# Performance work log

Hardware: AMD Instinct MI355X
Metric: run time of the kernel (lower is better)

## Reference

```python
import jax, jax.numpy as jnp
import numpy as np

N_HEAD, D_MODEL, D_HEAD, D_OUT = 16, 1024, 64, 1024
Q_INNER = N_HEAD * D_HEAD


def setup_inputs() -> dict:
    key = jax.random.key(0)
    ks = jax.random.split(key, 10)
    B, S = 1, 4096
    hidden_state = jax.random.normal(ks[0], (B, S, D_MODEL), dtype=jnp.float32)
    # causal mask, (B,1,S,S), 1 = attend, 0 = masked
    attention_mask = jnp.tril(jnp.ones((S, S), dtype=jnp.int32))[None, None, :, :]
    s = 0.02
    Wq = jax.random.normal(ks[1], (D_MODEL, Q_INNER), dtype=jnp.float32) * s
    bq = jnp.zeros((Q_INNER,), dtype=jnp.float32)
    Wk = jax.random.normal(ks[2], (D_MODEL, D_HEAD), dtype=jnp.float32) * s
    bk = jnp.zeros((D_HEAD,), dtype=jnp.float32)
    Wv = jax.random.normal(ks[3], (D_MODEL, D_HEAD), dtype=jnp.float32) * s
    bv = jnp.zeros((D_HEAD,), dtype=jnp.float32)
    Wo = jax.random.normal(ks[4], (Q_INNER, D_OUT), dtype=jnp.float32) * s
    bo = jnp.zeros((D_OUT,), dtype=jnp.float32)
    return {"hidden_state": hidden_state, "attention_mask": attention_mask,
            "Wq": Wq, "bq": bq, "Wk": Wk, "bk": bk, "Wv": Wv, "bv": bv,
            "Wo": Wo, "bo": bo}


def reference(hidden_state, attention_mask, Wq, bq, Wk, bk, Wv, bv, Wo, bo):
    B, S, _ = hidden_state.shape
    q = hidden_state @ Wq + bq                    # (B,S,H*Dh)
    k = hidden_state @ Wk + bk                    # (B,S,Dh) single shared KV head
    v = hidden_state @ Wv + bv                    # (B,S,Dh)
    q = q.reshape(B, S, N_HEAD, D_HEAD)           # (B,S,H,Dh)
    scale = 1.0 / jnp.sqrt(jnp.float32(D_HEAD))
    # scores: (B,H,S,S) — shared K broadcast over heads
    scores = jnp.einsum('bqhd,bkd->bhqk', q, k) * scale
    scores = jnp.where(attention_mask == 0, -jnp.inf, scores)
    probs = jax.nn.softmax(scores, axis=-1)
    out = jnp.einsum('bhqk,bkd->bqhd', probs, v)  # (B,S,H,Dh)
    out = out.reshape(B, S, Q_INNER)
    return out @ Wo + bo
```

## Files before the change

kernel.cpp:

```cpp
#include <hip/hip_runtime.h>
#include <hip/hip_bf16.h>
#include <math.h>

typedef __bf16 bf16;
typedef __bf16 bf16x4 __attribute__((ext_vector_type(4)));
typedef __bf16 bf16x8 __attribute__((ext_vector_type(8)));
typedef float f32x4 __attribute__((ext_vector_type(4)));

#define AS1(p) ((const __attribute__((address_space(1))) void*)(p))
#define AS3(p) ((__attribute__((address_space(3))) void*)(p))

__device__ __forceinline__ void gld_lds16(const void* g, void* l) {
  __builtin_amdgcn_global_load_lds(AS1(g), AS3(l), 16, 0, 0);
}

#define MFMA16(a, b, c) __builtin_amdgcn_mfma_f32_16x16x32_bf16((a), (b), (c), 0, 0, 0)

#define QSCALE_F 0.180336880f

struct Sched { unsigned short e[768]; };
constexpr Sched make_sched() {
  Sched s{};
  for (int bx = 0; bx < 256; ++bx) {
    int h = bx >> 4, i = bx & 15;
    s.e[bx]       = (unsigned short)(((31 - i) << 6) | (h << 2) | 1);
    s.e[bx + 256] = (unsigned short)(((31 - i) << 6) | (h << 2) | 2);
    s.e[bx + 512] = (unsigned short)((i << 6) | (h << 2) | 0);
  }
  return s;
}
__device__ constexpr Sched SCHED = make_sched();

__global__ void cast_f32_bf16(const float4* __restrict__ in, bf16* __restrict__ out, int n4) {
  int i = blockIdx.x * blockDim.x + threadIdx.x;
  if (i < n4) {
    float4 v = in[i];
    bf16x4 o4 = {(bf16)v.x, (bf16)v.y, (bf16)v.z, (bf16)v.w};
    *(bf16x4*)(out + (size_t)i * 4) = o4;
  }
}

__global__ void prep_wqkv(const float* __restrict__ Wq, const float* __restrict__ Wk,
                          const float* __restrict__ Wv, bf16* __restrict__ out) {
  __shared__ float t[64][65];
  const int ob = blockIdx.y;
  const float* src;
  int C, c0;
  if (ob < 16)      { src = Wq; C = 1024; c0 = ob * 64; }
  else if (ob == 16){ src = Wk; C = 64;   c0 = 0; }
  else              { src = Wv; C = 64;   c0 = 0; }
  const int r0 = blockIdx.x * 64;
  const int tx = threadIdx.x & 63, ty = threadIdx.x >> 6;
#pragma unroll
  for (int j = 0; j < 16; j++)
    t[ty + j * 4][tx] = src[(size_t)(r0 + ty + j * 4) * C + c0 + tx];
  __syncthreads();
#pragma unroll
  for (int j = 0; j < 16; j++)
    out[(size_t)(ob * 64 + ty + j * 4) * 1024 + r0 + tx] = (bf16)t[tx][ty + j * 4];
}

__global__ void transpose_cast_f32_bf16(const float* __restrict__ in, bf16* __restrict__ out,
                                        int C, int ldout) {
  __shared__ float t[64][65];
  int r0 = blockIdx.y * 64, c0 = blockIdx.x * 64;
  int tx = threadIdx.x & 63, ty = threadIdx.x >> 6;
#pragma unroll
  for (int j = 0; j < 16; j++)
    t[ty + j * 4][tx] = in[(size_t)(r0 + ty + j * 4) * C + c0 + tx];
  __syncthreads();
#pragma unroll
  for (int j = 0; j < 16; j++)
    out[(size_t)(c0 + ty + j * 4) * ldout + r0 + tx] = (bf16)t[tx][ty + j * 4];
}

__global__ void pack_bias3(const float* __restrict__ bq, const float* __restrict__ bk,
                           const float* __restrict__ bv, float* __restrict__ o) {
  int i = blockIdx.x * 256 + threadIdx.x;
  if (i < 1024) o[i] = bq[i];
  else if (i < 1088) o[i] = bk[i - 1024];
  else if (i < 1152) o[i] = bv[i - 1088];
}

template <int OUTF32, int QSCALE>
__global__ __launch_bounds__(256) void gemm_bt64(const bf16* __restrict__ A,
                                                 const bf16* __restrict__ B,
                                                 const float* __restrict__ bias,
                                                 void* __restrict__ Cout,
                                                 int M, int N, int K) {
  __shared__ bf16 As[64 * 32];
  __shared__ bf16 Bs[128 * 32];
  const int tid = threadIdx.x, w = tid >> 6, lane = tid & 63;
  const int g = lane >> 4, r = lane & 15;
  const int cpx = gridDim.x >> 3;
  const int l = (blockIdx.x & 7) * cpx + (blockIdx.x >> 3);
  const int ntn = N >> 7;
  const int my = l / ntn, mx = l - my * ntn;
  const int tm = my * 64, tn = mx * 128;
  const int wr = w >> 1, wc = w & 1;

  f32x4 acc[2][4] = {};

  const char* gA = (const char*)(A + (size_t)tm * K);
  const char* gB = (const char*)(B + (size_t)tn * K);
  const int linA = w * 1024 + lane * 16;
  const int lin0 = (w * 2 + 0) * 1024 + lane * 16;
  const int lin1 = (w * 2 + 1) * 1024 + lane * 16;
  const int rA = linA >> 6, cA = linA & 63;
  const int rB0 = lin0 >> 6, cB0 = lin0 & 63;
  const int rB1 = lin1 >> 6, cB1 = lin1 & 63;
  char* ldsA  = (char*)As + w * 1024;
  char* ldsB0 = (char*)Bs + (w * 2 + 0) * 1024;
  char* ldsB1 = (char*)Bs + (w * 2 + 1) * 1024;

  for (int k0 = 0; k0 < K; k0 += 32) {
    gld_lds16(gA + (size_t)rA * (K * 2) + k0 * 2 + cA, ldsA);
    gld_lds16(gB + (size_t)rB0 * (K * 2) + k0 * 2 + cB0, ldsB0);
    gld_lds16(gB + (size_t)rB1 * (K * 2) + k0 * 2 + cB1, ldsB1);
    __syncthreads();

    bf16x8 af[2], bfr[4];
#pragma unroll
    for (int m = 0; m < 2; m++)
      af[m] = *(const bf16x8*)&As[(wr * 32 + m * 16 + r) * 32 + g * 8];
#pragma unroll
    for (int n = 0; n < 4; n++)
      bfr[n] = *(const bf16x8*)&Bs[(wc * 64 + n * 16 + r) * 32 + g * 8];
#pragma unroll
    for (int m = 0; m < 2; m++)
#pragma unroll
      for (int n = 0; n < 4; n++)
        acc[m][n] = MFMA16(af[m], bfr[n], acc[m][n]);
    __syncthreads();
  }

#pragma unroll
  for (int m = 0; m < 2; m++) {
#pragma unroll
    for (int n = 0; n < 4; n++) {
      int crow = tm + wr * 32 + m * 16 + g * 4;
      int ccol = tn + wc * 64 + n * 16 + r;
      float bb = bias[ccol];
      float sc = (QSCALE && ccol < 1024) ? QSCALE_F : 1.0f;
#pragma unroll
      for (int j = 0; j < 4; j++) {
        float v = (acc[m][n][j] + bb) * sc;
        if (OUTF32)
          ((float*)Cout)[(size_t)(crow + j) * N + ccol] = v;
        else
          ((bf16*)Cout)[(size_t)(crow + j) * N + ccol] = (bf16)v;
      }
    }
  }
}

__global__ void kv_prep(const bf16* __restrict__ QKV, bf16* __restrict__ Ksw,
                        bf16* __restrict__ Vtsw) {
  __shared__ bf16 Vld[64][72];
  const int kv0 = blockIdx.x * 64;
  const int tid = threadIdx.x;
#pragma unroll
  for (int cc = 0; cc < 2; cc++) {
    const int c = tid + cc * 256;
    const int kvl = c >> 3, c8 = c & 7;
    bf16x8 kv8 = *(const bf16x8*)(QKV + (size_t)(kv0 + kvl) * 1152 + 1024 + c8 * 8);
    *(bf16x8*)(Ksw + (size_t)(kv0 + kvl) * 64 + ((c8 * 8) ^ ((kvl & 7) << 3))) = kv8;
    bf16x8 vv = *(const bf16x8*)(QKV + (size_t)(kv0 + kvl) * 1152 + 1088 + c8 * 8);
#pragma unroll
    for (int e = 0; e < 8; e++) Vld[c8 * 8 + e][kvl] = vv[e];
  }
  __syncthreads();
#pragma unroll
  for (int cc = 0; cc < 2; cc++) {
    const int c = tid + cc * 256;
    const int d = c >> 3, k8 = c & 7;
    bf16x8 o8 = *(const bf16x8*)&Vld[d][k8 * 8];
    *(bf16x8*)(Vtsw + (size_t)d * 4096 + kv0 + ((k8 * 8) ^ ((d & 7) << 3))) = o8;
  }
}

__global__ __launch_bounds__(256) void mqa_fwd(const bf16* __restrict__ QKV,
                                               const bf16* __restrict__ Ksw,
                                               const bf16* __restrict__ Vtsw,
                                               bf16* __restrict__ AO,
                                               float* __restrict__ po,
                                               float* __restrict__ psum) {
  __shared__ bf16 Ks[2][64 * 64];
  __shared__ bf16 Vs[2][64 * 64];
  __shared__ bf16 Ps[4 * 32 * 64];

  const int e = SCHED.e[blockIdx.x];
  const int qt = e >> 6, h = (e >> 2) & 15, part = e & 3;
  const int tbeg = (part == 2) ? qt + 1 : 0;
  const int tend = (part == 1) ? qt + 1 : 2 * qt + 2;

  const int tid = threadIdx.x, w = tid >> 6, lane = tid & 63;
  const int g = lane >> 4, r = lane & 15;
  const int qw = qt * 128 + w * 32;
  const int qown0 = qw + r;
  const int qown1 = qw + 16 + r;

  const char* Kg = (const char*)Ksw;
  const char* Vg = (const char*)Vtsw;
  char* PsB = (char*)Ps;
  const int lin0 = w * 2048 + lane * 16;
  const int lin1 = lin0 + 1024;
  const int sz = (r & 7) << 4;

  bf16x8 qf0[2], qf1[2];
#pragma unroll
  for (int kk = 0; kk < 2; kk++) {
    qf0[kk] = *(const bf16x8*)&QKV[(size_t)qown0 * 1152 + h * 64 + kk * 32 + g * 8];
    qf1[kk] = *(const bf16x8*)&QKV[(size_t)qown1 * 1152 + h * 64 + kk * 32 + g * 8];
  }

  const bf16 one = (bf16)1.0f;
  const bf16x8 ones = {one, one, one, one, one, one, one, one};

  f32x4 o[2][4] = {};
  f32x4 sums[2] = {};

  auto STAGE = [&](int t, int b) {
    const int kn = t * 64;
    char* kb = (char*)Ks + b * 8192 + w * 2048;
    char* vb = (char*)Vs + b * 8192 + w * 2048;
    gld_lds16(Kg + (size_t)kn * 128 + lin0, kb);
    gld_lds16(Kg + (size_t)kn * 128 + lin1, kb + 1024);
    gld_lds16(Vg + (size_t)(lin0 >> 7) * 8192 + kn * 2 + (lin0 & 127), vb);
    gld_lds16(Vg + (size_t)(lin1 >> 7) * 8192 + kn * 2 + (lin1 & 127), vb + 1024);
  };

  int buf = 0;
  STAGE(tbeg, 0);
  for (int t = tbeg; t < tend; ++t) {
    if (t + 1 < tend) {
      STAGE(t + 1, buf ^ 1);
      asm volatile("s_waitcnt vmcnt(4)" ::: "memory");
    } else {
      asm volatile("s_waitcnt vmcnt(0)" ::: "memory");
    }
    __builtin_amdgcn_sched_barrier(0);
    __builtin_amdgcn_s_barrier();

    const char* kt = (const char*)Ks + buf * 8192;
    const char* vt = (const char*)Vs + buf * 8192;
    const int kv0 = t * 64;

    f32x4 s0[4], s1[4];
    __builtin_amdgcn_s_setprio(1);
#pragma unroll
    for (int n = 0; n < 4; n++) {
      bf16x8 kf0 = *(const bf16x8*)(kt + (n * 16 + r) * 128 + ((g * 16) ^ sz));
      bf16x8 kf1 = *(const bf16x8*)(kt + (n * 16 + r) * 128 + ((64 + g * 16) ^ sz));
      f32x4 z0 = {0.f, 0.f, 0.f, 0.f};
      z0 = MFMA16(kf0, qf0[0], z0);
      z0 = MFMA16(kf1, qf0[1], z0);
      s0[n] = z0;
      f32x4 z1 = {0.f, 0.f, 0.f, 0.f};
      z1 = MFMA16(kf0, qf1[0], z1);
      z1 = MFMA16(kf1, qf1[1], z1);
      s1[n] = z1;
    }
    __builtin_amdgcn_s_setprio(0);

    if (t >= 2 * qt) {
#pragma unroll
      for (int n = 0; n < 4; n++)
#pragma unroll
        for (int jj = 0; jj < 4; jj++) {
          const int kv = kv0 + n * 16 + g * 4 + jj;
          if (kv > qown0) s0[n][jj] = -3.0e38f;
          if (kv > qown1) s1[n][jj] = -3.0e38f;
        }
    }

#pragma unroll
    for (int n = 0; n < 4; n++) {
      bf16x4 pk0, pk1;
#pragma unroll
      for (int jj = 0; jj < 4; jj++) {
        pk0[jj] = (bf16)__builtin_amdgcn_exp2f(s0[n][jj]);
        pk1[jj] = (bf16)__builtin_amdgcn_exp2f(s1[n][jj]);
      }
      *(bf16x4*)(PsB + w * 4096 + r * 128 + ((n * 32 + g * 8) ^ sz)) = pk0;
      *(bf16x4*)(PsB + w * 4096 + (16 + r) * 128 + ((n * 32 + g * 8) ^ sz)) = pk1;
    }

    asm volatile("s_waitcnt lgkmcnt(0)" ::: "memory");
    __builtin_amdgcn_sched_barrier(0);

    bf16x8 pa00 = *(const bf16x8*)(PsB + w * 4096 + r * 128 + ((g * 16) ^ sz));
    bf16x8 pa01 = *(const bf16x8*)(PsB + w * 4096 + r * 128 + ((64 + g * 16) ^ sz));
    bf16x8 pa10 = *(const bf16x8*)(PsB + w * 4096 + (16 + r) * 128 + ((g * 16) ^ sz));
    bf16x8 pa11 = *(const bf16x8*)(PsB + w * 4096 + (16 + r) * 128 + ((64 + g * 16) ^ sz));
    __builtin_amdgcn_s_setprio(1);
    sums[0] = MFMA16(pa00, ones, sums[0]);
    sums[0] = MFMA16(pa01, ones, sums[0]);
    sums[1] = MFMA16(pa10, ones, sums[1]);
    sums[1] = MFMA16(pa11, ones, sums[1]);
#pragma unroll
    for (int n = 0; n < 4; n++) {
      bf16x8 vf0 = *(const bf16x8*)(vt + (n * 16 + r) * 128 + ((g * 16) ^ sz));
      bf16x8 vf1 = *(const bf16x8*)(vt + (n * 16 + r) * 128 + ((64 + g * 16) ^ sz));
      o[0][n] = MFMA16(pa00, vf0, o[0][n]);
      o[0][n] = MFMA16(pa01, vf1, o[0][n]);
      o[1][n] = MFMA16(pa10, vf0, o[1][n]);
      o[1][n] = MFMA16(pa11, vf1, o[1][n]);
    }
    __builtin_amdgcn_s_setprio(0);
    __builtin_amdgcn_s_barrier();
    buf ^= 1;
  }

  if (part == 0) {
#pragma unroll
    for (int H = 0; H < 2; H++)
#pragma unroll
      for (int jj = 0; jj < 4; jj++) {
        const float inv = 1.f / sums[H][jj];
        const int row = qw + H * 16 + g * 4 + jj;
#pragma unroll
        for (int n = 0; n < 4; n++)
          AO[(size_t)row * 1024 + h * 64 + n * 16 + r] = (bf16)(o[H][n][jj] * inv);
      }
  } else {
    const int slot = ((qt - 16) * 16 + h) * 2 + (part - 1);
    float* pb = po + (size_t)slot * 8192;
#pragma unroll
    for (int H = 0; H < 2; H++)
#pragma unroll
      for (int jj = 0; jj < 4; jj++) {
        const int row = w * 32 + H * 16 + g * 4 + jj;
#pragma unroll
        for (int n = 0; n < 4; n++)
          pb[row * 64 + n * 16 + r] = o[H][n][jj];
        if (r == 0) psum[slot * 128 + row] = sums[H][jj];
      }
  }
}

__global__ __launch_bounds__(256) void combine_split(const float* __restrict__ po,
                                                     const float* __restrict__ psum,
                                                     bf16* __restrict__ AO) {
  const int bxx = blockIdx.x;
  const int qt = 16 + (bxx >> 4), h = bxx & 15;
  const float* a  = po + (size_t)bxx * 16384;
  const float* b  = a + 8192;
  const float* sa = psum + bxx * 256;
  const float* sb = sa + 128;
  const int row = threadIdx.x >> 1, c0 = (threadIdx.x & 1) * 32;
  const float inv = 1.f / (sa[row] + sb[row]);
  const float* pa = a + row * 64 + c0;
  const float* pb = b + row * 64 + c0;
  bf16* dst = AO + (size_t)(qt * 128 + row) * 1024 + h * 64 + c0;
#pragma unroll
  for (int i = 0; i < 8; i++) {
    float4 va = ((const float4*)pa)[i];
    float4 vb = ((const float4*)pb)[i];
    bf16x4 o4 = {(bf16)((va.x + vb.x) * inv), (bf16)((va.y + vb.y) * inv),
                 (bf16)((va.z + vb.z) * inv), (bf16)((va.w + vb.w) * inv)};
    ((bf16x4*)dst)[i] = o4;
  }
}

extern "C" void kernel_launch(void* const* d_in, const int* in_sizes, int n_in,
                              void* d_out, int out_size, void* d_ws, size_t ws_size,
                              hipStream_t stream) {
  const float* H  = (const float*)d_in[0];
  const float* Wq = (const float*)d_in[2];
  const float* bq = (const float*)d_in[3];
  const float* Wk = (const float*)d_in[4];
  const float* bk = (const float*)d_in[5];
  const float* Wv = (const float*)d_in[6];
  const float* bv = (const float*)d_in[7];
  const float* Wo = (const float*)d_in[8];
  const float* bo = (const float*)d_in[9];
  float* out = (float*)d_out;

  const int S = 4096, DM = 1024;

  char* p = (char*)d_ws;
  bf16* Hb    = (bf16*)(p);
  bf16* QKV   = (bf16*)(p + 8388608);
  bf16* Wqkvt = (bf16*)(p + 17825792);
  bf16* Wot   = (bf16*)(p + 20185088);
  float* bqkv = (float*)(p + 22282240);
  bf16* Ksw   = (bf16*)(p + 22286848);
  bf16* Vtsw  = (bf16*)(p + 22811136);
  float* po   = (float*)(p + 23335424);
  float* psum = (float*)(p + 40112640);
  bf16* AOb   = Hb;

  cast_f32_bf16<<<(S * DM / 4 + 255) / 256, 256, 0, stream>>>((const float4*)H, Hb, S * DM / 4);
  prep_wqkv<<<dim3(16, 18), 256, 0, stream>>>(Wq, Wk, Wv, Wqkvt);
  transpose_cast_f32_bf16<<<dim3(16, 16), 256, 0, stream>>>(Wo, Wot, 1024, 1024);
  pack_bias3<<<5, 256, 0, stream>>>(bq, bk, bv, bqkv);

  gemm_bt64<0, 1><<<576, 256, 0, stream>>>(Hb, Wqkvt, bqkv, QKV, S, 1152, 1024);

  kv_prep<<<64, 256, 0, stream>>>(QKV, Ksw, Vtsw);

  mqa_fwd<<<768, 256, 0, stream>>>(QKV, Ksw, Vtsw, AOb, po, psum);
  combine_split<<<256, 256, 0, stream>>>(po, psum, AOb);

  gemm_bt64<1, 0><<<512, 256, 0, stream>>>(AOb, Wot, bo, out, S, 1024, 1024);
}
```

Baseline: 125.4 us.

## Balance causal attention work with tape schedule, double-buffer GEMM, bf16 partials

Replaces the fixed three-way split schedule with a compile-time tape. Each of the 768 blocks processes up to two segments, drawn from a paired short/long query tile, so that every block covers at most 22 KV tiles. The combine kernel now sums a variable number of partial slots (336 jobs). Partial outputs are stored as bf16 instead of fp32 to cut combine traffic, at some precision cost. Separately, the projection GEMM gains double-buffered LDS staging with async prefetch and MFMA priority hints, and fully-masked waves on the last diagonal tile skip compute.

```diff
diff --git a/kernel.cpp b/kernel.cpp
--- a/kernel.cpp
+++ b/kernel.cpp
@@ -18,18 +18,71 @@
 
 #define QSCALE_F 0.180336880f
 
-struct Sched { unsigned short e[768]; };
-constexpr Sched make_sched() {
-  Sched s{};
-  for (int bx = 0; bx < 256; ++bx) {
-    int h = bx >> 4, i = bx & 15;
-    s.e[bx]       = (unsigned short)(((31 - i) << 6) | (h << 2) | 1);
-    s.e[bx + 256] = (unsigned short)(((31 - i) << 6) | (h << 2) | 2);
-    s.e[bx + 512] = (unsigned short)((i << 6) | (h << 2) | 0);
-  }
-  return s;
-}
-__device__ constexpr Sched SCHED = make_sched();
+struct Seg { short qt, h, t0, t1, slot; };
+struct Tape { Seg s[768][2]; };
+struct CJob { short qt, h, base, parts; };
+struct CTab { CJob j[336]; };
+
+constexpr Tape make_tape() {
+  Tape tp{};
+  for (int b = 0; b < 768; ++b)
+    for (int s = 0; s < 2; ++s) tp.s[b][s] = Seg{0, 0, 0, 0, -1};
+  int slot_next = 0, blk = 0;
+  for (int h = 0; h < 16; ++h)
+    for (int i = 0; i < 16; ++i) {
+      const int n1 = 2 * i + 2;
+      const int qtj[2] = {i, 31 - i};
+      const int js[2] = {0, n1};
+      const int je[2] = {n1, 66};
+      int base[2] = {-1, -1}, fb[2] = {0, 0};
+      for (int j = 0; j < 2; ++j) {
+        fb[j] = js[j] / 22;
+        const int lb = (je[j] - 1) / 22;
+        const int parts = lb - fb[j] + 1;
+        if (parts > 1) { base[j] = slot_next; slot_next += parts; }
+      }
+      for (int k = 0; k < 3; ++k) {
+        int si = 0;
+        for (int j = 0; j < 2; ++j) {
+          const int a = js[j] > 22 * k ? js[j] : 22 * k;
+          const int b2 = je[j] < 22 * k + 22 ? je[j] : 22 * k + 22;
+          if (a < b2) {
+            const int slot = (base[j] >= 0) ? base[j] + (k - fb[j]) : -1;
+            tp.s[blk][si] = Seg{(short)qtj[j], (short)h, (short)(a - js[j]),
+                                (short)(b2 - js[j]), (short)slot};
+            ++si;
+          }
+        }
+        ++blk;
+      }
+    }
+  return tp;
+}
+
+constexpr CTab make_ctab() {
+  CTab ct{};
+  int slot_next = 0, nj = 0;
+  for (int h = 0; h < 16; ++h)
+    for (int i = 0; i < 16; ++i) {
+      const int n1 = 2 * i + 2;
+      const int qtj[2] = {i, 31 - i};
+      const int js[2] = {0, n1};
+      const int je[2] = {n1, 66};
+      for (int j = 0; j < 2; ++j) {
+        const int fb = js[j] / 22, lb = (je[j] - 1) / 22;
+        const int parts = lb - fb + 1;
+        if (parts > 1) {
+          ct.j[nj] = CJob{(short)qtj[j], (short)h, (short)slot_next, (short)parts};
+          slot_next += parts;
+          ++nj;
+        }
+      }
+    }
+  return ct;
+}
+
+__device__ constexpr Tape TAPE = make_tape();
+__device__ constexpr CTab CTAB = make_ctab();
 
 __global__ void cast_f32_bf16(const float4* __restrict__ in, bf16* __restrict__ out, int n4) {
   int i = blockIdx.x * blockDim.x + threadIdx.x;
@@ -88,8 +141,8 @@
                                                  const float* __restrict__ bias,
                                                  void* __restrict__ Cout,
                                                  int M, int N, int K) {
-  __shared__ bf16 As[64 * 32];
-  __shared__ bf16 Bs[128 * 32];
+  __shared__ bf16 As[2 * 64 * 32];
+  __shared__ bf16 Bs[2 * 128 * 32];
   const int tid = threadIdx.x, w = tid >> 6, lane = tid & 63;
   const int g = lane >> 4, r = lane & 15;
   const int cpx = gridDim.x >> 3;
@@ -109,29 +162,44 @@
   const int rA = linA >> 6, cA = linA & 63;
   const int rB0 = lin0 >> 6, cB0 = lin0 & 63;
   const int rB1 = lin1 >> 6, cB1 = lin1 & 63;
-  char* ldsA  = (char*)As + w * 1024;
-  char* ldsB0 = (char*)Bs + (w * 2 + 0) * 1024;
-  char* ldsB1 = (char*)Bs + (w * 2 + 1) * 1024;
-
-  for (int k0 = 0; k0 < K; k0 += 32) {
-    gld_lds16(gA + (size_t)rA * (K * 2) + k0 * 2 + cA, ldsA);
-    gld_lds16(gB + (size_t)rB0 * (K * 2) + k0 * 2 + cB0, ldsB0);
-    gld_lds16(gB + (size_t)rB1 * (K * 2) + k0 * 2 + cB1, ldsB1);
-    __syncthreads();
+
+  auto STAGE = [&](int ks, int b) {
+    char* dA = (char*)As + b * 4096 + w * 1024;
+    char* dB = (char*)Bs + b * 8192 + (w * 2) * 1024;
+    gld_lds16(gA + (size_t)rA * (K * 2) + ks * 64 + cA, dA);
+    gld_lds16(gB + (size_t)rB0 * (K * 2) + ks * 64 + cB0, dB);
+    gld_lds16(gB + (size_t)rB1 * (K * 2) + ks * 64 + cB1, dB + 1024);
+  };
+
+  const int nk = K >> 5;
+  STAGE(0, 0);
+  int buf = 0;
+  for (int ks = 0; ks < nk; ++ks) {
+    if (ks + 1 < nk) {
+      STAGE(ks + 1, buf ^ 1);
+      asm volatile("s_waitcnt vmcnt(3)" ::: "memory");
+    } else {
+      asm volatile("s_waitcnt vmcnt(0)" ::: "memory");
+    }
+    __builtin_amdgcn_sched_barrier(0);
+    __builtin_amdgcn_s_barrier();
 
     bf16x8 af[2], bfr[4];
 #pragma unroll
     for (int m = 0; m < 2; m++)
-      af[m] = *(const bf16x8*)&As[(wr * 32 + m * 16 + r) * 32 + g * 8];
+      af[m] = *(const bf16x8*)&As[buf * 2048 + (wr * 32 + m * 16 + r) * 32 + g * 8];
 #pragma unroll
     for (int n = 0; n < 4; n++)
-      bfr[n] = *(const bf16x8*)&Bs[(wc * 64 + n * 16 + r) * 32 + g * 8];
+      bfr[n] = *(const bf16x8*)&Bs[buf * 4096 + (wc * 64 + n * 16 + r) * 32 + g * 8];
+    __builtin_amdgcn_s_setprio(1);
 #pragma unroll
     for (int m = 0; m < 2; m++)
 #pragma unroll
       for (int n = 0; n < 4; n++)
         acc[m][n] = MFMA16(af[m], bfr[n], acc[m][n]);
-    __syncthreads();
+    __builtin_amdgcn_s_setprio(0);
+    __builtin_amdgcn_s_barrier();
+    buf ^= 1;
   }
 
 #pragma unroll
@@ -183,22 +251,14 @@
                                                const bf16* __restrict__ Ksw,
                                                const bf16* __restrict__ Vtsw,
                                                bf16* __restrict__ AO,
-                                               float* __restrict__ po,
+                                               bf16* __restrict__ po,
                                                float* __restrict__ psum) {
   __shared__ bf16 Ks[2][64 * 64];
   __shared__ bf16 Vs[2][64 * 64];
   __shared__ bf16 Ps[4 * 32 * 64];
 
-  const int e = SCHED.e[blockIdx.x];
-  const int qt = e >> 6, h = (e >> 2) & 15, part = e & 3;
-  const int tbeg = (part == 2) ? qt + 1 : 0;
-  const int tend = (part == 1) ? qt + 1 : 2 * qt + 2;
-
   const int tid = threadIdx.x, w = tid >> 6, lane = tid & 63;
   const int g = lane >> 4, r = lane & 15;
-  const int qw = qt * 128 + w * 32;
-  const int qown0 = qw + r;
-  const int qown1 = qw + 16 + r;
 
   const char* Kg = (const char*)Ksw;
   const char* Vg = (const char*)Vtsw;
@@ -207,18 +267,8 @@
   const int lin1 = lin0 + 1024;
   const int sz = (r & 7) << 4;
 
-  bf16x8 qf0[2], qf1[2];
-#pragma unroll
-  for (int kk = 0; kk < 2; kk++) {
-    qf0[kk] = *(const bf16x8*)&QKV[(size_t)qown0 * 1152 + h * 64 + kk * 32 + g * 8];
-    qf1[kk] = *(const bf16x8*)&QKV[(size_t)qown1 * 1152 + h * 64 + kk * 32 + g * 8];
-  }
-
   const bf16 one = (bf16)1.0f;
   const bf16x8 ones = {one, one, one, one, one, one, one, one};
-
-  f32x4 o[2][4] = {};
-  f32x4 sums[2] = {};
 
   auto STAGE = [&](int t, int b) {
     const int kn = t * 64;
@@ -230,136 +280,164 @@
     gld_lds16(Vg + (size_t)(lin1 >> 7) * 8192 + kn * 2 + (lin1 & 127), vb + 1024);
   };
 
-  int buf = 0;
-  STAGE(tbeg, 0);
-  for (int t = tbeg; t < tend; ++t) {
-    if (t + 1 < tend) {
-      STAGE(t + 1, buf ^ 1);
-      asm volatile("s_waitcnt vmcnt(4)" ::: "memory");
+#pragma unroll 1
+  for (int sidx = 0; sidx < 2; ++sidx) {
+    const Seg sg = TAPE.s[blockIdx.x][sidx];
+    if (sg.t1 <= sg.t0) continue;
+    const int qt = sg.qt, h = sg.h, tbeg = sg.t0, tend = sg.t1, slot = sg.slot;
+    const int qw = qt * 128 + w * 32;
+    const int qown0 = qw + r;
+    const int qown1 = qw + 16 + r;
+
+    bf16x8 qf0[2], qf1[2];
+#pragma unroll
+    for (int kk = 0; kk < 2; kk++) {
+      qf0[kk] = *(const bf16x8*)&QKV[(size_t)qown0 * 1152 + h * 64 + kk * 32 + g * 8];
+      qf1[kk] = *(const bf16x8*)&QKV[(size_t)qown1 * 1152 + h * 64 + kk * 32 + g * 8];
+    }
+
+    f32x4 o[2][4] = {};
+    f32x4 sums[2] = {};
+
+    int buf = 0;
+    STAGE(tbeg, 0);
+#pragma unroll 1
+    for (int t = tbeg; t < tend; ++t) {
+      if (t + 1 < tend) {
+        STAGE(t + 1, buf ^ 1);
+        asm volatile("s_waitcnt vmcnt(4)" ::: "memory");
+      } else {
+        asm volatile("s_waitcnt vmcnt(0)" ::: "memory");
+      }
+      __builtin_amdgcn_sched_barrier(0);
+      __builtin_amdgcn_s_barrier();
+
+      const char* kt = (const char*)Ks + buf * 8192;
+      const char* vt = (const char*)Vs + buf * 8192;
+      const int kv0 = t * 64;
+      const bool deadw = (t == 2 * qt + 1) && (w < 2);
+
+      if (!deadw) {
+        f32x4 s0[4], s1[4];
+        __builtin_amdgcn_s_setprio(1);
+#pragma unroll
+        for (int n = 0; n < 4; n++) {
+          bf16x8 kf0 = *(const bf16x8*)(kt + (n * 16 + r) * 128 + ((g * 16) ^ sz));
+          bf16x8 kf1 = *(const bf16x8*)(kt + (n * 16 + r) * 128 + ((64 + g * 16) ^ sz));
+          f32x4 z0 = {0.f, 0.f, 0.f, 0.f};
+          z0 = MFMA16(kf0, qf0[0], z0);
+          z0 = MFMA16(kf1, qf0[1], z0);
+          s0[n] = z0;
+          f32x4 z1 = {0.f, 0.f, 0.f, 0.f};
+          z1 = MFMA16(kf0, qf1[0], z1);
+          z1 = MFMA16(kf1, qf1[1], z1);
+          s1[n] = z1;
+        }
+        __builtin_amdgcn_s_setprio(0);
+
+        if (t >= 2 * qt) {
+#pragma unroll
+          for (int n = 0; n < 4; n++)
+#pragma unroll
+            for (int jj = 0; jj < 4; jj++) {
+              const int kv = kv0 + n * 16 + g * 4 + jj;
+              if (kv > qown0) s0[n][jj] = -3.0e38f;
+              if (kv > qown1) s1[n][jj] = -3.0e38f;
+            }
+        }
+
+#pragma unroll
+        for (int n = 0; n < 4; n++) {
+          bf16x4 pk0, pk1;
+#pragma unroll
+          for (int jj = 0; jj < 4; jj++) {
+            pk0[jj] = (bf16)__builtin_amdgcn_exp2f(s0[n][jj]);
+            pk1[jj] = (bf16)__builtin_amdgcn_exp2f(s1[n][jj]);
+          }
+          *(bf16x4*)(PsB + w * 4096 + r * 128 + ((n * 32 + g * 8) ^ sz)) = pk0;
+          *(bf16x4*)(PsB + w * 4096 + (16 + r) * 128 + ((n * 32 + g * 8) ^ sz)) = pk1;
+        }
+
+        asm volatile("s_waitcnt lgkmcnt(0)" ::: "memory");
+        __builtin_amdgcn_sched_barrier(0);
+
+        bf16x8 pa00 = *(const bf16x8*)(PsB + w * 4096 + r * 128 + ((g * 16) ^ sz));
+        bf16x8 pa01 = *(const bf16x8*)(PsB + w * 4096 + r * 128 + ((64 + g * 16) ^ sz));
+        bf16x8 pa10 = *(const bf16x8*)(PsB + w * 4096 + (16 + r) * 128 + ((g * 16) ^ sz));
+        bf16x8 pa11 = *(const bf16x8*)(PsB + w * 4096 + (16 + r) * 128 + ((64 + g * 16) ^ sz));
+        __builtin_amdgcn_s_setprio(1);
+        sums[0] = MFMA16(pa00, ones, sums[0]);
+        sums[0] = MFMA16(pa01, ones, sums[0]);
+        sums[1] = MFMA16(pa10, ones, sums[1]);
+        sums[1] = MFMA16(pa11, ones, sums[1]);
+#pragma unroll
+        for (int n = 0; n < 4; n++) {
+          bf16x8 vf0 = *(const bf16x8*)(vt + (n * 16 + r) * 128 + ((g * 16) ^ sz));
+          bf16x8 vf1 = *(const bf16x8*)(vt + (n * 16 + r) * 128 + ((64 + g * 16) ^ sz));
+          o[0][n] = MFMA16(pa00, vf0, o[0][n]);
+          o[0][n] = MFMA16(pa01, vf1, o[0][n]);
+          o[1][n] = MFMA16(pa10, vf0, o[1][n]);
+          o[1][n] = MFMA16(pa11, vf1, o[1][n]);
+        }
+        __builtin_amdgcn_s_setprio(0);
+      }
+      __builtin_amdgcn_s_barrier();
+      buf ^= 1;
+    }
+
+    if (slot < 0) {
+#pragma unroll
+      for (int H = 0; H < 2; H++)
+#pragma unroll
+        for (int jj = 0; jj < 4; jj++) {
+          const float inv = 1.f / sums[H][jj];
+          const int row = qw + H * 16 + g * 4 + jj;
+#pragma unroll
+          for (int n = 0; n < 4; n++)
+            AO[(size_t)row * 1024 + h * 64 + n * 16 + r] = (bf16)(o[H][n][jj] * inv);
+        }
     } else {
-      asm volatile("s_waitcnt vmcnt(0)" ::: "memory");
-    }
-    __builtin_amdgcn_sched_barrier(0);
-    __builtin_amdgcn_s_barrier();
-
-    const char* kt = (const char*)Ks + buf * 8192;
-    const char* vt = (const char*)Vs + buf * 8192;
-    const int kv0 = t * 64;
-
-    f32x4 s0[4], s1[4];
-    __builtin_amdgcn_s_setprio(1);
-#pragma unroll
-    for (int n = 0; n < 4; n++) {
-      bf16x8 kf0 = *(const bf16x8*)(kt + (n * 16 + r) * 128 + ((g * 16) ^ sz));
-      bf16x8 kf1 = *(const bf16x8*)(kt + (n * 16 + r) * 128 + ((64 + g * 16) ^ sz));
-      f32x4 z0 = {0.f, 0.f, 0.f, 0.f};
-      z0 = MFMA16(kf0, qf0[0], z0);
-      z0 = MFMA16(kf1, qf0[1], z0);
-      s0[n] = z0;
-      f32x4 z1 = {0.f, 0.f, 0.f, 0.f};
-      z1 = MFMA16(kf0, qf1[0], z1);
-      z1 = MFMA16(kf1, qf1[1], z1);
-      s1[n] = z1;
-    }
-    __builtin_amdgcn_s_setprio(0);
-
-    if (t >= 2 * qt) {
-#pragma unroll
-      for (int n = 0; n < 4; n++)
+      bf16* pb = po + (size_t)slot * 8192;
+#pragma unroll
+      for (int H = 0; H < 2; H++)
 #pragma unroll
         for (int jj = 0; jj < 4; jj++) {
-          const int kv = kv0 + n * 16 + g * 4 + jj;
-          if (kv > qown0) s0[n][jj] = -3.0e38f;
-          if (kv > qown1) s1[n][jj] = -3.0e38f;
-        }
-    }
-
-#pragma unroll
-    for (int n = 0; n < 4; n++) {
-      bf16x4 pk0, pk1;
-#pragma unroll
-      for (int jj = 0; jj < 4; jj++) {
-        pk0[jj] = (bf16)__builtin_amdgcn_exp2f(s0[n][jj]);
-        pk1[jj] = (bf16)__builtin_amdgcn_exp2f(s1[n][jj]);
-      }
-      *(bf16x4*)(PsB + w * 4096 + r * 128 + ((n * 32 + g * 8) ^ sz)) = pk0;
-      *(bf16x4*)(PsB + w * 4096 + (16 + r) * 128 + ((n * 32 + g * 8) ^ sz)) = pk1;
-    }
-
-    asm volatile("s_waitcnt lgkmcnt(0)" ::: "memory");
-    __builtin_amdgcn_sched_barrier(0);
-
-    bf16x8 pa00 = *(const bf16x8*)(PsB + w * 4096 + r * 128 + ((g * 16) ^ sz));
-    bf16x8 pa01 = *(const bf16x8*)(PsB + w * 4096 + r * 128 + ((64 + g * 16) ^ sz));
-    bf16x8 pa10 = *(const bf16x8*)(PsB + w * 4096 + (16 + r) * 128 + ((g * 16) ^ sz));
-    bf16x8 pa11 = *(const bf16x8*)(PsB + w * 4096 + (16 + r) * 128 + ((64 + g * 16) ^ sz));
-    __builtin_amdgcn_s_setprio(1);
-    sums[0] = MFMA16(pa00, ones, sums[0]);
-    sums[0] = MFMA16(pa01, ones, sums[0]);
-    sums[1] = MFMA16(pa10, ones, sums[1]);
-    sums[1] = MFMA16(pa11, ones, sums[1]);
-#pragma unroll
-    for (int n = 0; n < 4; n++) {
-      bf16x8 vf0 = *(const bf16x8*)(vt + (n * 16 + r) * 128 + ((g * 16) ^ sz));
-      bf16x8 vf1 = *(const bf16x8*)(vt + (n * 16 + r) * 128 + ((64 + g * 16) ^ sz));
-      o[0][n] = MFMA16(pa00, vf0, o[0][n]);
-      o[0][n] = MFMA16(pa01, vf1, o[0][n]);
-      o[1][n] = MFMA16(pa10, vf0, o[1][n]);
-      o[1][n] = MFMA16(pa11, vf1, o[1][n]);
-    }
-    __builtin_amdgcn_s_setprio(0);
-    __builtin_amdgcn_s_barrier();
-    buf ^= 1;
-  }
-
-  if (part == 0) {
-#pragma unroll
-    for (int H = 0; H < 2; H++)
-#pragma unroll
-      for (int jj = 0; jj < 4; jj++) {
-        const float inv = 1.f / sums[H][jj];
-        const int row = qw + H * 16 + g * 4 + jj;
-#pragma unroll
-        for (int n = 0; n < 4; n++)
-          AO[(size_t)row * 1024 + h * 64 + n * 16 + r] = (bf16)(o[H][n][jj] * inv);
-      }
-  } else {
-    const int slot = ((qt - 16) * 16 + h) * 2 + (part - 1);
-    float* pb = po + (size_t)slot * 8192;
-#pragma unroll
-    for (int H = 0; H < 2; H++)
-#pragma unroll
-      for (int jj = 0; jj < 4; jj++) {
-        const int row = w * 32 + H * 16 + g * 4 + jj;
-#pragma unroll
-        for (int n = 0; n < 4; n++)
-          pb[row * 64 + n * 16 + r] = o[H][n][jj];
-        if (r == 0) psum[slot * 128 + row] = sums[H][jj];
-      }
-  }
-}
-
-__global__ __launch_bounds__(256) void combine_split(const float* __restrict__ po,
+          const int row = w * 32 + H * 16 + g * 4 + jj;
+#pragma unroll
+          for (int n = 0; n < 4; n++)
+            pb[row * 64 + n * 16 + r] = (bf16)o[H][n][jj];
+          if (r == 0) psum[slot * 128 + row] = sums[H][jj];
+        }
+    }
+  }
+}
+
+__global__ __launch_bounds__(256) void combine_split(const bf16* __restrict__ po,
                                                      const float* __restrict__ psum,
                                                      bf16* __restrict__ AO) {
-  const int bxx = blockIdx.x;
-  const int qt = 16 + (bxx >> 4), h = bxx & 15;
-  const float* a  = po + (size_t)bxx * 16384;
-  const float* b  = a + 8192;
-  const float* sa = psum + bxx * 256;
-  const float* sb = sa + 128;
+  const CJob cj = CTAB.j[blockIdx.x];
   const int row = threadIdx.x >> 1, c0 = (threadIdx.x & 1) * 32;
-  const float inv = 1.f / (sa[row] + sb[row]);
-  const float* pa = a + row * 64 + c0;
-  const float* pb = b + row * 64 + c0;
-  bf16* dst = AO + (size_t)(qt * 128 + row) * 1024 + h * 64 + c0;
-#pragma unroll
-  for (int i = 0; i < 8; i++) {
-    float4 va = ((const float4*)pa)[i];
-    float4 vb = ((const float4*)pb)[i];
-    bf16x4 o4 = {(bf16)((va.x + vb.x) * inv), (bf16)((va.y + vb.y) * inv),
-                 (bf16)((va.z + vb.z) * inv), (bf16)((va.w + vb.w) * inv)};
-    ((bf16x4*)dst)[i] = o4;
+  float acc[32] = {};
+  float ssum = 0.f;
+#pragma unroll 1
+  for (int p = 0; p < cj.parts; ++p) {
+    const bf16* pb = po + (size_t)(cj.base + p) * 8192 + row * 64 + c0;
+    ssum += psum[(cj.base + p) * 128 + row];
+#pragma unroll
+    for (int v = 0; v < 4; ++v) {
+      bf16x8 x = ((const bf16x8*)pb)[v];
+#pragma unroll
+      for (int e = 0; e < 8; e++) acc[v * 8 + e] += (float)x[e];
+    }
+  }
+  const float inv = 1.f / ssum;
+  bf16* dst = AO + (size_t)(cj.qt * 128 + row) * 1024 + cj.h * 64 + c0;
+#pragma unroll
+  for (int v = 0; v < 4; ++v) {
+    bf16x8 oo;
+#pragma unroll
+    for (int e = 0; e < 8; e++) oo[e] = (bf16)(acc[v * 8 + e] * inv);
+    ((bf16x8*)dst)[v] = oo;
   }
 }
 
@@ -387,8 +465,8 @@
   float* bqkv = (float*)(p + 22282240);
   bf16* Ksw   = (bf16*)(p + 22286848);
   bf16* Vtsw  = (bf16*)(p + 22811136);
-  float* po   = (float*)(p + 23335424);
-  float* psum = (float*)(p + 40112640);
+  bf16* po    = (bf16*)(p + 23335424);
+  float* psum = (float*)(p + 36966912);
   bf16* AOb   = Hb;
 
   cast_f32_bf16<<<(S * DM / 4 + 255) / 256, 256, 0, stream>>>((const float4*)H, Hb, S * DM / 4);
@@ -401,7 +479,7 @@
   kv_prep<<<64, 256, 0, stream>>>(QKV, Ksw, Vtsw);
 
   mqa_fwd<<<768, 256, 0, stream>>>(QKV, Ksw, Vtsw, AOb, po, psum);
-  combine_split<<<256, 256, 0, stream>>>(po, psum, AOb);
+  combine_split<<<336, 256, 0, stream>>>(po, psum, AOb);
 
   gemm_bt64<1, 0><<<512, 256, 0, stream>>>(AOb, Wot, bo, out, S, 1024, 1024);
 }
```

Result: slower. 132.5 us (+5.7%).
